# Performance work log

Measured on AMD Instinct MI355X. Metric: run time of the kernel, lower is better.

## Reference

```python
import jax, jax.numpy as jnp
import numpy as np

B, N, TAU = 2, 256, 32
ELLS = [0, 1, 2, 3]  # m-dim sizes 1,3,5,7


def setup_inputs() -> dict:
    key = jax.random.key(0)
    ks = jax.random.split(key, len(ELLS))
    inp = {}
    for i, ell in enumerate(ELLS):
        inp[f"rep{ell}"] = jax.random.normal(ks[i], (B, N, TAU, 2 * ell + 1, 2), dtype=jnp.float32)
    return inp


def _dot_part(part, ell):
    # part: [B, N, tau, m, 2] with m = 2*ell+1, trailing dim = (real, imag)
    dt = part.dtype
    # signs = (-1)^k for k in [-ell, ell]; use parity to avoid negative float powers
    signs = jnp.where(jnp.arange(-ell, ell + 1) % 2 == 0, 1.0, -1.0).astype(dt)  # (m,)
    conj = jnp.array([1.0, -1.0], dtype=dt)  # (2,)
    # part2 = flip over m, multiplied by signs (the SO3 conjugation of the second factor)
    p2 = jnp.flip(part, axis=-2) * signs[:, None]  # [B, N, tau, m, 2]
    # real part: sum_m sum_c part1[i] * p2[j] * conj[c]  -> [B, N_i, N_j, tau]
    dot_r = jnp.einsum('bitmc,bjtmc,c->bijt', part, p2, conj)
    # imag part: contract part1 against p2 with real/imag swapped
    dot_i = jnp.einsum('bitmc,bjtmc->bijt', part, jnp.flip(p2, axis=-1))
    return jnp.stack([dot_r, dot_i], axis=-1)  # [B, N, N, tau, 2]


def reference(rep0, rep1, rep2, rep3):
    parts = [rep0, rep1, rep2, rep3]
    dots = [_dot_part(p, ell) for ell, p in enumerate(parts)]
    # cat=True: concatenate channel (tau) axis over all ell.
    # The torch module returns this same tensor replicated len(reps) times;
    # we return the single concatenated tensor.
    return jnp.concatenate(dots, axis=-2)  # [B, N, N, sum(tau), 2]
```

## Files before the change

kernel.cpp:

```cpp
#include <hip/hip_runtime.h>


namespace {

constexpr int Bn = 2;
constexpr int Nn = 256;
constexpr int TAUn = 32;
constexpr int TI = 16;
constexpr int TJ = 16;
constexpr int OUTPAIR = 2 * 4 * TAUn;

template <int ELL>
__device__ __forceinline__ void dot_ell(const float* __restrict__ rep,
                                        float* __restrict__ out,
                                        int b, int i0, int j0, int tid,
                                        float* lds) {
  constexpr int M = 2 * ELL + 1;
  constexpr int RF = TAUn * M * 2;

  const float4* gA4 = reinterpret_cast<const float4*>(rep + (size_t)(b * Nn + i0) * RF);
  float4* lds4 = reinterpret_cast<float4*>(lds);
  constexpr int N4 = TI * RF / 4;
  for (int k = tid; k < N4; k += 256) lds4[k] = gA4[k];
  __syncthreads();

  const int tausub = tid & 7;
  const int slot   = tid >> 3;
  const int jj     = slot & 15;
  const int i0s    = slot >> 4;

  const float* gB = rep + (size_t)(b * Nn + j0 + jj) * RF + tausub * 4 * (2 * M);
  float w[4][M][2];
  #pragma unroll
  for (int q = 0; q < 4; ++q) {
    #pragma unroll
    for (int m = 0; m < M; ++m) {
      const float s = ((m ^ ELL) & 1) ? -1.0f : 1.0f;
      w[q][m][0] = gB[q * 2 * M + (2 * ELL - m) * 2 + 0] * s;
      w[q][m][1] = gB[q * 2 * M + (2 * ELL - m) * 2 + 1] * s;
    }
  }

  #pragma unroll
  for (int it = 0; it < 8; ++it) {
    const int ii = i0s + 2 * it;
    const float* la = lds + ii * RF + tausub * 4 * (2 * M);
    float res[8];
    #pragma unroll
    for (int q = 0; q < 4; ++q) {
      float dr = 0.0f, di = 0.0f;
      #pragma unroll
      for (int m = 0; m < M; ++m) {
        const float ar = la[q * 2 * M + 2 * m];
        const float ai = la[q * 2 * M + 2 * m + 1];
        dr = fmaf(ar, w[q][m][0], dr);
        dr = fmaf(-ai, w[q][m][1], dr);
        di = fmaf(ar, w[q][m][1], di);
        di = fmaf(ai, w[q][m][0], di);
      }
      res[2 * q]     = dr;
      res[2 * q + 1] = di;
    }
    float* op = out + (size_t)((b * Nn + i0 + ii) * Nn + (j0 + jj)) * OUTPAIR
                + ELL * 64 + tausub * 8;
    reinterpret_cast<float4*>(op)[0] = make_float4(res[0], res[1], res[2], res[3]);
    reinterpret_cast<float4*>(op)[1] = make_float4(res[4], res[5], res[6], res[7]);
  }
}

__global__ __launch_bounds__(256) void dotmat_kernel(
    const float* __restrict__ r0, const float* __restrict__ r1,
    const float* __restrict__ r2, const float* __restrict__ r3,
    float* __restrict__ out) {
  __shared__ __align__(16) float lds[TI * TAUn * 7 * 2];
  const int bz  = blockIdx.z;
  const int b   = bz >> 2;
  const int ell = bz & 3;
  const int i0  = blockIdx.y * TI;
  const int j0  = blockIdx.x * TJ;
  const int tid = threadIdx.x;
  switch (ell) {
    case 0: dot_ell<0>(r0, out, b, i0, j0, tid, lds); break;
    case 1: dot_ell<1>(r1, out, b, i0, j0, tid, lds); break;
    case 2: dot_ell<2>(r2, out, b, i0, j0, tid, lds); break;
    case 3: dot_ell<3>(r3, out, b, i0, j0, tid, lds); break;
  }
}

}

extern "C" void kernel_launch(void* const* d_in, const int* in_sizes, int n_in,
                              void* d_out, int out_size, void* d_ws, size_t ws_size,
                              hipStream_t stream) {
  (void)in_sizes; (void)n_in; (void)out_size; (void)d_ws; (void)ws_size;
  const float* r0 = (const float*)d_in[0];
  const float* r1 = (const float*)d_in[1];
  const float* r2 = (const float*)d_in[2];
  const float* r3 = (const float*)d_in[3];
  float* out = (float*)d_out;
  dim3 grid(Nn / TJ, Nn / TI, Bn * 4);
  dotmat_kernel<<<grid, 256, 0, stream>>>(r0, r1, r2, r3, out);
}
```

Measured before the change: 165.7 us.

## Fuse all ell levels per block for contiguous output rows with nontemporal stores

Each block now handles all four ell values for one batch over an 8x16 (i,j) tile, replacing the previous one-ell-per-block layout. Every thread writes 16-byte chunks into all four ell segments, so each (i,j) output row of 256 floats is written whole by one block rather than scattered across four blocks. The stores use nontemporal hints to stream the large output past the caches. In exchange, LDS use per block grows, registers rise because weights for every ell are held at once, and each thread does more work per output row.

```diff
diff --git a/kernel.cpp b/kernel.cpp
--- a/kernel.cpp
+++ b/kernel.cpp
@@ -3,87 +3,104 @@
 
 namespace {
 
+typedef float f32x4 __attribute__((ext_vector_type(4)));
+
 constexpr int Bn = 2;
 constexpr int Nn = 256;
-constexpr int TAUn = 32;
-constexpr int TI = 16;
+constexpr int TI = 8;
 constexpr int TJ = 16;
-constexpr int OUTPAIR = 2 * 4 * TAUn;
+
+__host__ __device__ constexpr int rf(int ell) { return 32 * (2 * ell + 1) * 2; }
+
+constexpr int OFF0 = 0;
+constexpr int OFF1 = OFF0 + TI * 64;
+constexpr int OFF2 = OFF1 + TI * 192;
+constexpr int OFF3 = OFF2 + TI * 320;
+constexpr int LDSF = OFF3 + TI * 448;
+
+__device__ __forceinline__ void stage(const float* __restrict__ src,
+                                      float* __restrict__ dst, int nf, int tid) {
+  const f32x4* s4 = reinterpret_cast<const f32x4*>(src);
+  f32x4* d4 = reinterpret_cast<f32x4*>(dst);
+  for (int k = tid; k < nf / 4; k += 256) d4[k] = s4[k];
+}
 
 template <int ELL>
-__device__ __forceinline__ void dot_ell(const float* __restrict__ rep,
-                                        float* __restrict__ out,
-                                        int b, int i0, int j0, int tid,
-                                        float* lds) {
+__device__ __forceinline__ void load_w(const float* __restrict__ rep, int b, int jg,
+                                       int f, float (&w)[2][2 * ELL + 1][2]) {
   constexpr int M = 2 * ELL + 1;
-  constexpr int RF = TAUn * M * 2;
-
-  const float4* gA4 = reinterpret_cast<const float4*>(rep + (size_t)(b * Nn + i0) * RF);
-  float4* lds4 = reinterpret_cast<float4*>(lds);
-  constexpr int N4 = TI * RF / 4;
-  for (int k = tid; k < N4; k += 256) lds4[k] = gA4[k];
-  __syncthreads();
-
-  const int tausub = tid & 7;
-  const int slot   = tid >> 3;
-  const int jj     = slot & 15;
-  const int i0s    = slot >> 4;
-
-  const float* gB = rep + (size_t)(b * Nn + j0 + jj) * RF + tausub * 4 * (2 * M);
-  float w[4][M][2];
+  const float* g = rep + (size_t)(b * Nn + jg) * rf(ELL) + (2 * f) * (2 * M);
   #pragma unroll
-  for (int q = 0; q < 4; ++q) {
+  for (int t = 0; t < 2; ++t) {
     #pragma unroll
     for (int m = 0; m < M; ++m) {
       const float s = ((m ^ ELL) & 1) ? -1.0f : 1.0f;
-      w[q][m][0] = gB[q * 2 * M + (2 * ELL - m) * 2 + 0] * s;
-      w[q][m][1] = gB[q * 2 * M + (2 * ELL - m) * 2 + 1] * s;
+      w[t][m][0] = g[t * 2 * M + (2 * ELL - m) * 2 + 0] * s;
+      w[t][m][1] = g[t * 2 * M + (2 * ELL - m) * 2 + 1] * s;
     }
   }
+}
 
+template <int ELL>
+__device__ __forceinline__ f32x4 dot2(const float* __restrict__ la,
+                                      const float (&w)[2][2 * ELL + 1][2]) {
+  constexpr int M = 2 * ELL + 1;
+  float r[2][2];
   #pragma unroll
-  for (int it = 0; it < 8; ++it) {
-    const int ii = i0s + 2 * it;
-    const float* la = lds + ii * RF + tausub * 4 * (2 * M);
-    float res[8];
+  for (int t = 0; t < 2; ++t) { r[t][0] = 0.0f; r[t][1] = 0.0f; }
+  #pragma unroll
+  for (int t = 0; t < 2; ++t) {
     #pragma unroll
-    for (int q = 0; q < 4; ++q) {
-      float dr = 0.0f, di = 0.0f;
-      #pragma unroll
-      for (int m = 0; m < M; ++m) {
-        const float ar = la[q * 2 * M + 2 * m];
-        const float ai = la[q * 2 * M + 2 * m + 1];
-        dr = fmaf(ar, w[q][m][0], dr);
-        dr = fmaf(-ai, w[q][m][1], dr);
-        di = fmaf(ar, w[q][m][1], di);
-        di = fmaf(ai, w[q][m][0], di);
-      }
-      res[2 * q]     = dr;
-      res[2 * q + 1] = di;
+    for (int m = 0; m < M; ++m) {
+      const float ar = la[t * 2 * M + 2 * m + 0];
+      const float ai = la[t * 2 * M + 2 * m + 1];
+      r[t][0] = fmaf(ar, w[t][m][0], r[t][0]);
+      r[t][0] = fmaf(-ai, w[t][m][1], r[t][0]);
+      r[t][1] = fmaf(ar, w[t][m][1], r[t][1]);
+      r[t][1] = fmaf(ai, w[t][m][0], r[t][1]);
     }
-    float* op = out + (size_t)((b * Nn + i0 + ii) * Nn + (j0 + jj)) * OUTPAIR
-                + ELL * 64 + tausub * 8;
-    reinterpret_cast<float4*>(op)[0] = make_float4(res[0], res[1], res[2], res[3]);
-    reinterpret_cast<float4*>(op)[1] = make_float4(res[4], res[5], res[6], res[7]);
   }
+  f32x4 v;
+  v.x = r[0][0]; v.y = r[0][1]; v.z = r[1][0]; v.w = r[1][1];
+  return v;
 }
 
 __global__ __launch_bounds__(256) void dotmat_kernel(
     const float* __restrict__ r0, const float* __restrict__ r1,
     const float* __restrict__ r2, const float* __restrict__ r3,
     float* __restrict__ out) {
-  __shared__ __align__(16) float lds[TI * TAUn * 7 * 2];
-  const int bz  = blockIdx.z;
-  const int b   = bz >> 2;
-  const int ell = bz & 3;
-  const int i0  = blockIdx.y * TI;
-  const int j0  = blockIdx.x * TJ;
+  __shared__ __align__(16) float lds[LDSF];
+  const int b  = blockIdx.z;
+  const int i0 = blockIdx.y * TI;
+  const int j0 = blockIdx.x * TJ;
   const int tid = threadIdx.x;
-  switch (ell) {
-    case 0: dot_ell<0>(r0, out, b, i0, j0, tid, lds); break;
-    case 1: dot_ell<1>(r1, out, b, i0, j0, tid, lds); break;
-    case 2: dot_ell<2>(r2, out, b, i0, j0, tid, lds); break;
-    case 3: dot_ell<3>(r3, out, b, i0, j0, tid, lds); break;
+
+  stage(r0 + (size_t)(b * Nn + i0) * 64,  lds + OFF0, TI * 64,  tid);
+  stage(r1 + (size_t)(b * Nn + i0) * 192, lds + OFF1, TI * 192, tid);
+  stage(r2 + (size_t)(b * Nn + i0) * 320, lds + OFF2, TI * 320, tid);
+  stage(r3 + (size_t)(b * Nn + i0) * 448, lds + OFF3, TI * 448, tid);
+
+  const int f  = tid & 15;
+  const int jj = tid >> 4;
+
+  float w0[2][1][2], w1[2][3][2], w2[2][5][2], w3[2][7][2];
+  load_w<0>(r0, b, j0 + jj, f, w0);
+  load_w<1>(r1, b, j0 + jj, f, w1);
+  load_w<2>(r2, b, j0 + jj, f, w2);
+  load_w<3>(r3, b, j0 + jj, f, w3);
+
+  __syncthreads();
+
+  for (int it = 0; it < TI; ++it) {
+    float* op = out + (size_t)((b * Nn + i0 + it) * Nn + (j0 + jj)) * 256 + f * 4;
+    const f32x4 v0 = dot2<0>(lds + OFF0 + it * 64  + (2 * f) * 2,  w0);
+    const f32x4 v1 = dot2<1>(lds + OFF1 + it * 192 + (2 * f) * 6,  w1);
+    const f32x4 v2 = dot2<2>(lds + OFF2 + it * 320 + (2 * f) * 10, w2);
+    const f32x4 v3 = dot2<3>(lds + OFF3 + it * 448 + (2 * f) * 14, w3);
+    __builtin_nontemporal_store(v0, reinterpret_cast<f32x4*>(op + 0 * 64));
+    __builtin_nontemporal_store(v1, reinterpret_cast<f32x4*>(op + 1 * 64));
+    __builtin_nontemporal_store(v2, reinterpret_cast<f32x4*>(op + 2 * 64));
+    __builtin_nontemporal_store(v3, reinterpret_cast<f32x4*>(op + 3 * 64));
   }
 }
 
@@ -98,6 +115,6 @@
   const float* r2 = (const float*)d_in[2];
   const float* r3 = (const float*)d_in[3];
   float* out = (float*)d_out;
-  dim3 grid(Nn / TJ, Nn / TI, Bn * 4);
+  dim3 grid(Nn / TJ, Nn / TI, Bn);
   dotmat_kernel<<<grid, 256, 0, stream>>>(r0, r1, r2, r3, out);
 }
```

Result: faster. 150.8 us (-9.0%).
